# Kernel optimization log

Hardware: AMD Instinct MI355X
Metric: run time of the kernel (lower is better)

The kernel has to match this reference:

```python
import jax, jax.numpy as jnp
import numpy as np
import math

TAU = 0.05
N_ITERS = 10
LR = 1.0
BETA1 = 0.9
BETA2 = 0.999
EPS_ADAM = 1e-08

BATCH, N, M = 8, 1024, 1024


def setup_inputs() -> dict:
    key = jax.random.key(0)
    log_alpha = jax.random.normal(key, (BATCH, N, M), dtype=jnp.float32)
    return {"log_alpha": log_alpha}


def reference(log_alpha):
    batch, n, m = log_alpha.shape
    dtype = log_alpha.dtype
    # default uniform log-marginals (log_a = -log n, log_b = -log m)
    log_a = jnp.full((batch, n), -math.log(float(n)), dtype=dtype)
    log_b = jnp.full((batch, m), -math.log(float(m)), dtype=dtype)
    # schedule=None -> tau constant, so the kernel is loop-invariant
    kernel = log_alpha / TAU  # [B, N, M]

    def step(carry, iter_idx):
        u, v, m_u, v_u, m_v, v_v = carry
        t = (iter_idx + 1).astype(dtype)
        bc1 = 1.0 - jnp.power(jnp.asarray(BETA1, dtype), t)
        bc2 = 1.0 - jnp.power(jnp.asarray(BETA2, dtype), t)

        # u half-step
        u_target = log_a - jax.nn.logsumexp(kernel + v[:, None, :], axis=-1)
        g_u = u_target - u
        m_u = BETA1 * m_u + (1.0 - BETA1) * g_u
        v_u = BETA2 * v_u + (1.0 - BETA2) * (g_u * g_u)
        u_next = u + LR * (m_u / bc1) / (jnp.sqrt(v_u / bc2) + EPS_ADAM)

        # v half-step (uses u_next, as in the torch loop)
        v_target = log_b - jax.nn.logsumexp(kernel + u_next[:, :, None], axis=-2)
        g_v = v_target - v
        m_v = BETA1 * m_v + (1.0 - BETA1) * g_v
        v_v = BETA2 * v_v + (1.0 - BETA2) * (g_v * g_v)
        v_next = v + LR * (m_v / bc1) / (jnp.sqrt(v_v / bc2) + EPS_ADAM)

        return (u_next, v_next, m_u, v_u, m_v, v_v), None

    z_n = jnp.zeros((batch, n), dtype=dtype)
    z_m = jnp.zeros((batch, m), dtype=dtype)
    init = (z_n, z_m, z_n, z_n, z_m, z_m)
    (u, v, _, _, _, _), _ = jax.lax.scan(step, init, jnp.arange(N_ITERS))

    # final transport plan at the target tau
    plan = jnp.exp(kernel + u[:, :, None] + v[:, None, :])
    return plan
```

## Files before the change

### kernel.cpp

```cpp
#include <hip/hip_runtime.h>
#include <math.h>

#define INV_TAU   20.0f
#define LOGN      6.931471805599453f
#define B1        0.9f
#define B2        0.999f
#define EPS_ADAM  1e-8f

constexpr int BATCH = 8;
constexpr int N = 1024;
constexpr int M = 1024;
constexpr int NITER = 10;
constexpr int CHUNKS = 64;
constexpr int PMSTRIDE = BATCH * M;

__device__ inline float max4f(float4 a) {
  return fmaxf(fmaxf(a.x, a.y), fmaxf(a.z, a.w));
}

__global__ __launch_bounds__(256) void k_init(float* __restrict__ p) {
  p[blockIdx.x * 256 + threadIdx.x] = 0.f;
}

__global__ __launch_bounds__(512, 4) void k_iter(
    const float* __restrict__ la, const float* __restrict__ vg,
    float* __restrict__ u, float* __restrict__ mu, float* __restrict__ vu,
    float* __restrict__ pm, float* __restrict__ ps,
    float bc1, float bc2)
{
  __shared__ float  wred[16][4];
  __shared__ float  rowmax[16];
  __shared__ float  u_s[16];
  __shared__ float4 cmm4[256], css4[256];

  const int blk = blockIdx.x;
  const int b   = blk & 7;
  const int c   = blk >> 3;
  const int i0  = c * 16;
  const int tid = threadIdx.x;
  const int c4  = tid & 255;
  const int rg  = tid >> 8;
  const int wq  = (tid >> 6) & 3;
  const int lane = tid & 63;

  const float4* la4 = (const float4*)la;
  float4 y[8];
#pragma unroll
  for (int rr = 0; rr < 8; ++rr) {
    float4 t = la4[((size_t)(b * N + i0 + rg * 8 + rr) << 8) + c4];
    t.x *= INV_TAU; t.y *= INV_TAU; t.z *= INV_TAU; t.w *= INV_TAU;
    y[rr] = t;
  }
  float4 v4 = ((const float4*)(vg + b * M))[c4];

  float rv[8];
#pragma unroll
  for (int rr = 0; rr < 8; ++rr) {
    rv[rr] = max4f(make_float4(y[rr].x + v4.x, y[rr].y + v4.y,
                               y[rr].z + v4.z, y[rr].w + v4.w));
  }
#pragma unroll
  for (int off = 1; off < 64; off <<= 1) {
#pragma unroll
    for (int rr = 0; rr < 8; ++rr) rv[rr] = fmaxf(rv[rr], __shfl_xor(rv[rr], off));
  }
  if (lane == 0) {
#pragma unroll
    for (int rr = 0; rr < 8; ++rr) wred[rg * 8 + rr][wq] = rv[rr];
  }
  __syncthreads();
  if (tid < 16)
    rowmax[tid] = fmaxf(fmaxf(wred[tid][0], wred[tid][1]),
                        fmaxf(wred[tid][2], wred[tid][3]));
  __syncthreads();

#pragma unroll
  for (int rr = 0; rr < 8; ++rr) {
    float m = rowmax[rg * 8 + rr];
    rv[rr] = __expf(y[rr].x + v4.x - m) + __expf(y[rr].y + v4.y - m) +
             __expf(y[rr].z + v4.z - m) + __expf(y[rr].w + v4.w - m);
  }
#pragma unroll
  for (int off = 1; off < 64; off <<= 1) {
#pragma unroll
    for (int rr = 0; rr < 8; ++rr) rv[rr] += __shfl_xor(rv[rr], off);
  }
  if (lane == 0) {
#pragma unroll
    for (int rr = 0; rr < 8; ++rr) wred[rg * 8 + rr][wq] = rv[rr];
  }
  __syncthreads();

  if (tid < 16) {
    float s   = wred[tid][0] + wred[tid][1] + wred[tid][2] + wred[tid][3];
    int   gi  = b * N + i0 + tid;
    float lse = rowmax[tid] + __logf(s);
    float uo  = u[gi];
    float g   = (-LOGN - lse) - uo;
    float mn  = B1 * mu[gi] + (1.0f - B1) * g;
    float vn  = B2 * vu[gi] + (1.0f - B2) * g * g;
    mu[gi] = mn; vu[gi] = vn;
    float un = uo + (mn / bc1) / (sqrtf(vn / bc2) + EPS_ADAM);
    u[gi] = un; u_s[tid] = un;
  }
  __syncthreads();

  float4 xm = make_float4(-INFINITY, -INFINITY, -INFINITY, -INFINITY);
#pragma unroll
  for (int rr = 0; rr < 8; ++rr) {
    float uu = u_s[rg * 8 + rr];
    xm.x = fmaxf(xm.x, y[rr].x + uu); xm.y = fmaxf(xm.y, y[rr].y + uu);
    xm.z = fmaxf(xm.z, y[rr].z + uu); xm.w = fmaxf(xm.w, y[rr].w + uu);
  }
  float4 xs = make_float4(0.f, 0.f, 0.f, 0.f);
#pragma unroll
  for (int rr = 0; rr < 8; ++rr) {
    float uu = u_s[rg * 8 + rr];
    xs.x += __expf(y[rr].x + uu - xm.x); xs.y += __expf(y[rr].y + uu - xm.y);
    xs.z += __expf(y[rr].z + uu - xm.z); xs.w += __expf(y[rr].w + uu - xm.w);
  }
  if (rg == 1) { cmm4[c4] = xm; css4[c4] = xs; }
  __syncthreads();
  if (rg == 0) {
    float4 om = cmm4[c4], os = css4[c4], nm, ns;
    nm.x = fmaxf(xm.x, om.x); ns.x = xs.x * __expf(xm.x - nm.x) + os.x * __expf(om.x - nm.x);
    nm.y = fmaxf(xm.y, om.y); ns.y = xs.y * __expf(xm.y - nm.y) + os.y * __expf(om.y - nm.y);
    nm.z = fmaxf(xm.z, om.z); ns.z = xs.z * __expf(xm.z - nm.z) + os.z * __expf(om.z - nm.z);
    nm.w = fmaxf(xm.w, om.w); ns.w = xs.w * __expf(xm.w - nm.w) + os.w * __expf(om.w - nm.w);
    ((float4*)(pm + c * PMSTRIDE + b * M))[c4] = nm;
    ((float4*)(ps + c * PMSTRIDE + b * M))[c4] = ns;
  }
}

__global__ __launch_bounds__(256) void k_comb(
    const float* __restrict__ pm, const float* __restrict__ ps,
    float* __restrict__ vg, float* __restrict__ mv, float* __restrict__ vv,
    float bc1, float bc2)
{
  const int cx = blockIdx.x * 256 + threadIdx.x;
  float m0 = -INFINITY, s0 = 0.f, m1 = -INFINITY, s1 = 0.f;
  float m2 = -INFINITY, s2 = 0.f, m3 = -INFINITY, s3 = 0.f;
#pragma unroll
  for (int cn = 0; cn < CHUNKS; cn += 4) {
    float am, nm;
    am = pm[(cn + 0) * PMSTRIDE + cx]; nm = fmaxf(m0, am);
    s0 = s0 * __expf(m0 - nm) + ps[(cn + 0) * PMSTRIDE + cx] * __expf(am - nm); m0 = nm;
    am = pm[(cn + 1) * PMSTRIDE + cx]; nm = fmaxf(m1, am);
    s1 = s1 * __expf(m1 - nm) + ps[(cn + 1) * PMSTRIDE + cx] * __expf(am - nm); m1 = nm;
    am = pm[(cn + 2) * PMSTRIDE + cx]; nm = fmaxf(m2, am);
    s2 = s2 * __expf(m2 - nm) + ps[(cn + 2) * PMSTRIDE + cx] * __expf(am - nm); m2 = nm;
    am = pm[(cn + 3) * PMSTRIDE + cx]; nm = fmaxf(m3, am);
    s3 = s3 * __expf(m3 - nm) + ps[(cn + 3) * PMSTRIDE + cx] * __expf(am - nm); m3 = nm;
  }
  float nm01 = fmaxf(m0, m1);
  float s01  = s0 * __expf(m0 - nm01) + s1 * __expf(m1 - nm01);
  float nm23 = fmaxf(m2, m3);
  float s23  = s2 * __expf(m2 - nm23) + s3 * __expf(m3 - nm23);
  float Mx   = fmaxf(nm01, nm23);
  float S    = s01 * __expf(nm01 - Mx) + s23 * __expf(nm23 - Mx);

  float lse = Mx + __logf(S);
  float vo  = vg[cx];
  float g   = (-LOGN - lse) - vo;
  float mn  = B1 * mv[cx] + (1.0f - B1) * g;
  float vn  = B2 * vv[cx] + (1.0f - B2) * g * g;
  mv[cx] = mn; vv[cx] = vn;
  vg[cx] = vo + (mn / bc1) / (sqrtf(vn / bc2) + EPS_ADAM);
}

__global__ __launch_bounds__(256) void k_plan(
    const float* __restrict__ la, const float* __restrict__ u,
    const float* __restrict__ v, float* __restrict__ out)
{
  size_t idx = (size_t)blockIdx.x * 256 + threadIdx.x;
  int row = (int)(idx >> 8);
  int b   = row >> 10;
  int jc  = (int)(idx & 255);
  float ur  = u[row];
  float4 v4 = ((const float4*)(v + b * M))[jc];
  float4 k4 = ((const float4*)la)[idx];
  float4 o;
  o.x = __expf(fmaf(k4.x, INV_TAU, ur + v4.x));
  o.y = __expf(fmaf(k4.y, INV_TAU, ur + v4.y));
  o.z = __expf(fmaf(k4.z, INV_TAU, ur + v4.z));
  o.w = __expf(fmaf(k4.w, INV_TAU, ur + v4.w));
  ((float4*)out)[idx] = o;
}

extern "C" void kernel_launch(void* const* d_in, const int* in_sizes, int n_in,
                              void* d_out, int out_size, void* d_ws, size_t ws_size,
                              hipStream_t stream) {
  const float* la = (const float*)d_in[0];
  float* out = (float*)d_out;
  float* ws  = (float*)d_ws;

  float* u  = ws;
  float* v  = ws + 8192;
  float* mu = ws + 16384;
  float* vu = ws + 24576;
  float* mv = ws + 32768;
  float* vv = ws + 40960;
  float* pm = ws + 49152;
  float* ps = pm + CHUNKS * PMSTRIDE;

  k_init<<<192, 256, 0, stream>>>(ws);

  for (int it = 0; it < NITER; ++it) {
    float t = (float)(it + 1);
    float bc1 = 1.0f - powf(B1, t);
    float bc2 = 1.0f - powf(B2, t);
    k_iter<<<CHUNKS * BATCH, 512, 0, stream>>>(la, v, u, mu, vu, pm, ps, bc1, bc2);
    k_comb<<<(BATCH * M) / 256, 256, 0, stream>>>(pm, ps, v, mv, vv, bc1, bc2);
  }
  k_plan<<<(BATCH * N * M) / 4 / 256, 256, 0, stream>>>(la, u, v, out);
}
```

Before: 255.7 us.

## Parallelize chunk combine across threads and fold init into first iteration

The column combine kernel now splits the 64 partial max/sum chunks across 8 groups of threads per column. It merges them by shuffle and shared memory, so it launches 256 blocks instead of 32, raising parallelism for this latency-bound reduction. The separate zero-init kernel is removed and a 'first' flag makes the first iteration treat u, v and the Adam moments as zero, saving one launch. Launch bounds for k_iter are relaxed from 4 to 2 blocks per CU, which may change register allocation and occupancy.

```diff
diff --git a/kernel.cpp b/kernel.cpp
--- a/kernel.cpp
+++ b/kernel.cpp
@@ -18,15 +18,11 @@
   return fmaxf(fmaxf(a.x, a.y), fmaxf(a.z, a.w));
 }
 
-__global__ __launch_bounds__(256) void k_init(float* __restrict__ p) {
-  p[blockIdx.x * 256 + threadIdx.x] = 0.f;
-}
-
-__global__ __launch_bounds__(512, 4) void k_iter(
+__global__ __launch_bounds__(512, 2) void k_iter(
     const float* __restrict__ la, const float* __restrict__ vg,
     float* __restrict__ u, float* __restrict__ mu, float* __restrict__ vu,
     float* __restrict__ pm, float* __restrict__ ps,
-    float bc1, float bc2)
+    float bc1, float bc2, int first)
 {
   __shared__ float  wred[16][4];
   __shared__ float  rowmax[16];
@@ -51,7 +47,8 @@
     t.x *= INV_TAU; t.y *= INV_TAU; t.z *= INV_TAU; t.w *= INV_TAU;
     y[rr] = t;
   }
-  float4 v4 = ((const float4*)(vg + b * M))[c4];
+  float4 v4 = first ? make_float4(0.f, 0.f, 0.f, 0.f)
+                    : ((const float4*)(vg + b * M))[c4];
 
   float rv[8];
 #pragma unroll
@@ -95,10 +92,12 @@
     float s   = wred[tid][0] + wred[tid][1] + wred[tid][2] + wred[tid][3];
     int   gi  = b * N + i0 + tid;
     float lse = rowmax[tid] + __logf(s);
-    float uo  = u[gi];
+    float uo  = first ? 0.f : u[gi];
     float g   = (-LOGN - lse) - uo;
-    float mn  = B1 * mu[gi] + (1.0f - B1) * g;
-    float vn  = B2 * vu[gi] + (1.0f - B2) * g * g;
+    float mo  = first ? 0.f : mu[gi];
+    float vo  = first ? 0.f : vu[gi];
+    float mn  = B1 * mo + (1.0f - B1) * g;
+    float vn  = B2 * vo + (1.0f - B2) * g * g;
     mu[gi] = mn; vu[gi] = vn;
     float un = uo + (mn / bc1) / (sqrtf(vn / bc2) + EPS_ADAM);
     u[gi] = un; u_s[tid] = un;
@@ -135,37 +134,54 @@
 __global__ __launch_bounds__(256) void k_comb(
     const float* __restrict__ pm, const float* __restrict__ ps,
     float* __restrict__ vg, float* __restrict__ mv, float* __restrict__ vv,
-    float bc1, float bc2)
+    float bc1, float bc2, int first)
 {
-  const int cx = blockIdx.x * 256 + threadIdx.x;
-  float m0 = -INFINITY, s0 = 0.f, m1 = -INFINITY, s1 = 0.f;
-  float m2 = -INFINITY, s2 = 0.f, m3 = -INFINITY, s3 = 0.f;
-#pragma unroll
-  for (int cn = 0; cn < CHUNKS; cn += 4) {
-    float am, nm;
-    am = pm[(cn + 0) * PMSTRIDE + cx]; nm = fmaxf(m0, am);
-    s0 = s0 * __expf(m0 - nm) + ps[(cn + 0) * PMSTRIDE + cx] * __expf(am - nm); m0 = nm;
-    am = pm[(cn + 1) * PMSTRIDE + cx]; nm = fmaxf(m1, am);
-    s1 = s1 * __expf(m1 - nm) + ps[(cn + 1) * PMSTRIDE + cx] * __expf(am - nm); m1 = nm;
-    am = pm[(cn + 2) * PMSTRIDE + cx]; nm = fmaxf(m2, am);
-    s2 = s2 * __expf(m2 - nm) + ps[(cn + 2) * PMSTRIDE + cx] * __expf(am - nm); m2 = nm;
-    am = pm[(cn + 3) * PMSTRIDE + cx]; nm = fmaxf(m3, am);
-    s3 = s3 * __expf(m3 - nm) + ps[(cn + 3) * PMSTRIDE + cx] * __expf(am - nm); m3 = nm;
-  }
-  float nm01 = fmaxf(m0, m1);
-  float s01  = s0 * __expf(m0 - nm01) + s1 * __expf(m1 - nm01);
-  float nm23 = fmaxf(m2, m3);
-  float s23  = s2 * __expf(m2 - nm23) + s3 * __expf(m3 - nm23);
-  float Mx   = fmaxf(nm01, nm23);
-  float S    = s01 * __expf(nm01 - Mx) + s23 * __expf(nm23 - Mx);
-
-  float lse = Mx + __logf(S);
-  float vo  = vg[cx];
-  float g   = (-LOGN - lse) - vo;
-  float mn  = B1 * mv[cx] + (1.0f - B1) * g;
-  float vn  = B2 * vv[cx] + (1.0f - B2) * g * g;
-  mv[cx] = mn; vv[cx] = vn;
-  vg[cx] = vo + (mn / bc1) / (sqrtf(vn / bc2) + EPS_ADAM);
+  __shared__ float sm[4][32], ss[4][32];
+
+  const int tid  = threadIdx.x;
+  const int w    = tid >> 6;
+  const int lane = tid & 63;
+  const int col5 = lane & 31;
+  const int grp  = (w << 1) | (lane >> 5);
+  const int cx   = blockIdx.x * 32 + col5;
+
+  float m = -INFINITY, s = 0.f;
+#pragma unroll
+  for (int k = 0; k < 8; ++k) {
+    const int cn = (grp << 3) | k;
+    float am = pm[cn * PMSTRIDE + cx];
+    float as = ps[cn * PMSTRIDE + cx];
+    float nm = fmaxf(m, am);
+    s = s * __expf(m - nm) + as * __expf(am - nm); m = nm;
+  }
+  {
+    float om = __shfl_xor(m, 32);
+    float os = __shfl_xor(s, 32);
+    float nm = fmaxf(m, om);
+    s = s * __expf(m - nm) + os * __expf(om - nm); m = nm;
+  }
+  if (lane < 32) { sm[w][col5] = m; ss[w][col5] = s; }
+  __syncthreads();
+
+  if (tid < 32) {
+    float M0 = sm[0][tid], S0 = ss[0][tid];
+#pragma unroll
+    for (int ww = 1; ww < 4; ++ww) {
+      float om = sm[ww][tid], os = ss[ww][tid];
+      float nm = fmaxf(M0, om);
+      S0 = S0 * __expf(M0 - nm) + os * __expf(om - nm); M0 = nm;
+    }
+    const int gc  = blockIdx.x * 32 + tid;
+    float lse = M0 + __logf(S0);
+    float vo  = first ? 0.f : vg[gc];
+    float g   = (-LOGN - lse) - vo;
+    float mo  = first ? 0.f : mv[gc];
+    float vvo = first ? 0.f : vv[gc];
+    float mn  = B1 * mo + (1.0f - B1) * g;
+    float vn  = B2 * vvo + (1.0f - B2) * g * g;
+    mv[gc] = mn; vv[gc] = vn;
+    vg[gc] = vo + (mn / bc1) / (sqrtf(vn / bc2) + EPS_ADAM);
+  }
 }
 
 __global__ __launch_bounds__(256) void k_plan(
@@ -203,14 +219,15 @@
   float* pm = ws + 49152;
   float* ps = pm + CHUNKS * PMSTRIDE;
 
-  k_init<<<192, 256, 0, stream>>>(ws);
-
   for (int it = 0; it < NITER; ++it) {
     float t = (float)(it + 1);
     float bc1 = 1.0f - powf(B1, t);
     float bc2 = 1.0f - powf(B2, t);
-    k_iter<<<CHUNKS * BATCH, 512, 0, stream>>>(la, v, u, mu, vu, pm, ps, bc1, bc2);
-    k_comb<<<(BATCH * M) / 256, 256, 0, stream>>>(pm, ps, v, mv, vv, bc1, bc2);
+    int first = (it == 0) ? 1 : 0;
+    k_iter<<<CHUNKS * BATCH, 512, 0, stream>>>(la, v, u, mu, vu, pm, ps,
+                                               bc1, bc2, first);
+    k_comb<<<(BATCH * M) / 32, 256, 0, stream>>>(pm, ps, v, mv, vv,
+                                                 bc1, bc2, first);
   }
   k_plan<<<(BATCH * N * M) / 4 / 256, 256, 0, stream>>>(la, u, v, out);
 }
```

After: 239.8 us. -6.2%, faster.
